# Optimization experiments

Measured on AMD Instinct MI355X. Metric: run time of the kernel, lower is better.

## Reference

```python
import jax, jax.numpy as jnp
import numpy as np

N, E, K = 10000, 160000, 5
K3 = K ** 3  # 125 spline kernel entries (kernel_size=5, dim=3)
NUM_CLASSES = 6890
# 8 corner combinations of the degree-1 open B-spline in 3 dims
_COMBOS = jnp.asarray(np.array([[i, j, k] for i in (0, 1) for j in (0, 1) for k in (0, 1)], dtype=np.int32))


def spline_basis(pseudo):
    # pseudo: [E,3] in [0,1]; degree-1 open B-spline, kernel_size K per dim
    p = pseudo * (K - 1)
    lo_f = jnp.floor(p)
    frac = p - lo_f                                   # [E,3]
    lo = jnp.clip(lo_f.astype(jnp.int32), 0, K - 1)    # [E,3]
    hi = jnp.minimum(lo + 1, K - 1)
    w = jnp.stack([1.0 - frac, frac], axis=-1)         # [E,3,2]
    idx = jnp.stack([lo, hi], axis=-1)                 # [E,3,2]
    c = _COMBOS                                        # [8,3]
    b = w[:, 0, c[:, 0]] * w[:, 1, c[:, 1]] * w[:, 2, c[:, 2]]          # [E,8]
    flat = idx[:, 0, c[:, 0]] + K * idx[:, 1, c[:, 1]] + K * K * idx[:, 2, c[:, 2]]  # [E,8]
    return b, flat


def spline_conv(x, src, dst, b, flat, W, root, bias):
    # x: [N,in], W: [K3,in,out], root: [in,out], bias: [out]
    xW = jnp.einsum('ni,kio->nko', x, W)               # [N,K3,out]
    gathered = xW[src[:, None], flat]                  # [E,8,out]
    msg = jnp.einsum('es,eso->eo', b, gathered)        # [E,out]
    agg = jax.ops.segment_sum(msg, dst, num_segments=N)
    deg = jax.ops.segment_sum(jnp.ones((msg.shape[0],), msg.dtype), dst, num_segments=N)
    agg = agg / jnp.maximum(deg, 1.0)[:, None]         # mean aggregation
    return agg + x @ root + bias


def setup_inputs() -> dict:
    key = jax.random.key(0)
    ks = jax.random.split(key, 24)
    s = 0.1
    x = jax.random.normal(ks[0], (N, 1), jnp.float32)
    edge_index = jax.random.randint(ks[1], (2, E), 0, N)
    pseudo = jax.random.uniform(ks[2], (E, 3), dtype=jnp.float32)
    W1 = jax.random.normal(ks[3], (K3, 1, 32), jnp.float32) * s
    root1 = jax.random.normal(ks[4], (1, 32), jnp.float32) * s
    b1 = jnp.zeros((32,), jnp.float32)
    W2 = jax.random.normal(ks[5], (K3, 32, 64), jnp.float32) * s
    root2 = jax.random.normal(ks[6], (32, 64), jnp.float32) * s
    b2 = jnp.zeros((64,), jnp.float32)
    Ws = jax.random.normal(ks[7], (4, K3, 64, 64), jnp.float32) * s  # convs 3-6
    roots = jax.random.normal(ks[8], (4, 64, 64), jnp.float32) * s
    bs = jnp.zeros((4, 64), jnp.float32)
    lin1_w = jax.random.normal(ks[9], (64, 256), jnp.float32) * s
    lin1_b = jnp.zeros((256,), jnp.float32)
    lin2_w = jax.random.normal(ks[10], (256, NUM_CLASSES), jnp.float32) * s
    lin2_b = jnp.zeros((NUM_CLASSES,), jnp.float32)
    return {'x': x, 'edge_index': edge_index, 'pseudo': pseudo,
            'W1': W1, 'root1': root1, 'b1': b1,
            'W2': W2, 'root2': root2, 'b2': b2,
            'Ws': Ws, 'roots': roots, 'bs': bs,
            'lin1_w': lin1_w, 'lin1_b': lin1_b, 'lin2_w': lin2_w, 'lin2_b': lin2_b}


def reference(x, edge_index, pseudo, W1, root1, b1, W2, root2, b2, Ws, roots, bs,
              lin1_w, lin1_b, lin2_w, lin2_b):
    src, dst = edge_index[0], edge_index[1]
    b, flat = spline_basis(pseudo)
    h = jax.nn.elu(spline_conv(x, src, dst, b, flat, W1, root1, b1))
    h = jax.nn.elu(spline_conv(h, src, dst, b, flat, W2, root2, b2))
    for l in range(4):  # convs 3-6, fixed layer loop
        h = jax.nn.elu(spline_conv(h, src, dst, b, flat, Ws[l], roots[l], bs[l]))
    h = jax.nn.elu(h @ lin1_w + lin1_b)
    # dropout is identity in eval mode
    logits = h @ lin2_w + lin2_b
    return jax.nn.log_softmax(logits, axis=-1)
```

## Files before the change

### kernel.cpp

```cpp
#include <hip/hip_runtime.h>
#include <hip/hip_bf16.h>
#include <math.h>

#define Nn 10000
#define Ee 160000
#define NPB 40
#define NBLK 250
#define NKER 125
#define NBUCK (NBLK * NKER)
#define KCHUNK 32

#define MPAD 10048
#define NPAD 6912
#define NCLS 6890

typedef short bf16x8 __attribute__((ext_vector_type(8)));
typedef float f32x4  __attribute__((ext_vector_type(4)));

__global__ __launch_bounds__(256) void basis_kernel(const float* __restrict__ pseudo,
                                                    float* __restrict__ bw,
                                                    int* __restrict__ fl)
{
    int e = blockIdx.x * 256 + threadIdx.x;
    if (e >= Ee) return;
    float p0 = pseudo[e * 3 + 0] * 4.f;
    float p1 = pseudo[e * 3 + 1] * 4.f;
    float p2 = pseudo[e * 3 + 2] * 4.f;
    float f0 = floorf(p0), f1 = floorf(p1), f2 = floorf(p2);
    float fr0 = p0 - f0, fr1 = p1 - f1, fr2 = p2 - f2;
    int lo0 = (int)f0; lo0 = lo0 < 0 ? 0 : (lo0 > 4 ? 4 : lo0);
    int lo1 = (int)f1; lo1 = lo1 < 0 ? 0 : (lo1 > 4 ? 4 : lo1);
    int lo2 = (int)f2; lo2 = lo2 < 0 ? 0 : (lo2 > 4 ? 4 : lo2);
    int hi0 = lo0 + 1 > 4 ? 4 : lo0 + 1;
    int hi1 = lo1 + 1 > 4 ? 4 : lo1 + 1;
    int hi2 = lo2 + 1 > 4 ? 4 : lo2 + 1;
#pragma unroll
    for (int s = 0; s < 8; ++s) {
        int c0 = (s >> 2) & 1, c1 = (s >> 1) & 1, c2 = s & 1;
        float b = (c0 ? fr0 : 1.f - fr0) * (c1 ? fr1 : 1.f - fr1) * (c2 ? fr2 : 1.f - fr2);
        int f = (c0 ? hi0 : lo0) + 5 * (c1 ? hi1 : lo1) + 25 * (c2 ? hi2 : lo2);
        bw[e * 8 + s] = b;
        fl[e * 8 + s] = f;
    }
}

__global__ __launch_bounds__(256) void deg_kernel(const int* __restrict__ dst, int* __restrict__ degi)
{
    int e = blockIdx.x * 256 + threadIdx.x;
    if (e >= Ee) return;
    atomicAdd(&degi[dst[e]], 1);
}

__global__ __launch_bounds__(256) void invdeg_kernel(const int* __restrict__ degi, float* __restrict__ invdeg)
{
    int n = blockIdx.x * 256 + threadIdx.x;
    if (n >= Nn) return;
    int d = degi[n];
    invdeg[n] = 1.f / (float)(d > 0 ? d : 1);
}

__global__ __launch_bounds__(256) void hist_kernel(const int* __restrict__ dst, const int* __restrict__ fl,
                                                   int* __restrict__ hist)
{
    int t = blockIdx.x * 256 + threadIdx.x;
    if (t >= Ee * 8) return;
    int e = t >> 3;
    int key = (dst[e] / NPB) * NKER + fl[t];
    atomicAdd(&hist[key], 1);
}

__global__ __launch_bounds__(1024) void scan_kernel(const int* __restrict__ hist, int* __restrict__ boff)
{
    const int T = 1024;
    const int per = (NBUCK + T - 1) / T;
    int t = threadIdx.x;
    int beg = t * per;
    int end = beg + per; if (end > NBUCK) end = NBUCK;
    int s = 0;
    for (int i = beg; i < end && i < NBUCK; ++i) s += hist[i];
    __shared__ int tmp[1024];
    tmp[t] = s;
    __syncthreads();
    for (int o2 = 1; o2 < 1024; o2 <<= 1) {
        int v = (t >= o2) ? tmp[t - o2] : 0;
        __syncthreads();
        tmp[t] += v;
        __syncthreads();
    }
    int run = tmp[t] - s;
    for (int i = beg; i < end && i < NBUCK; ++i) { boff[i] = run; run += hist[i]; }
    if (t == T - 1) boff[NBUCK] = run;
}

__global__ __launch_bounds__(256) void fill_kernel(const int* __restrict__ srcA, const int* __restrict__ dstA,
                                                   const float* __restrict__ bw, const int* __restrict__ fl,
                                                   int* __restrict__ cursor, uint2* __restrict__ recs)
{
    int t = blockIdx.x * 256 + threadIdx.x;
    if (t >= Ee * 8) return;
    int e = t >> 3;
    int d = dstA[e];
    int key = (d / NPB) * NKER + fl[t];
    int pos = atomicAdd(&cursor[key], 1);
    unsigned meta = (unsigned)srcA[e] | ((unsigned)(d % NPB) << 16);
    recs[pos] = make_uint2(meta, __float_as_uint(bw[t]));
}

template <int CIN, int COUT>
__global__ __launch_bounds__(256) void conv_pairs_kernel(const uint2* __restrict__ recs,
                                                         const int* __restrict__ boff,
                                                         const float* __restrict__ xin,
                                                         const float* __restrict__ W,
                                                         float* __restrict__ agg)
{
    __shared__ float aggl[NPB * COUT];
    const int blk = blockIdx.x;
    for (int idx = threadIdx.x; idx < NPB * COUT; idx += 256) aggl[idx] = 0.f;
    __syncthreads();

    const int lane = threadIdx.x & 63;
    const int wid  = threadIdx.x >> 6;
    const int o    = lane;

    int k0 = blockIdx.y * KCHUNK;
    int k1 = k0 + KCHUNK; if (k1 > NKER) k1 = NKER;

    for (int k = k0 + wid; k < k1; k += 4) {
        int bidx = blk * NKER + k;
        int pb = boff[bidx], pe = boff[bidx + 1];
        if (pb >= pe) continue;
        float wreg[CIN];
#pragma unroll
        for (int i = 0; i < CIN; ++i)
            wreg[i] = (o < COUT) ? W[(k * CIN + i) * COUT + o] : 0.f;

        for (int p = pb; p < pe; ++p) {
            uint2 r = recs[p];
            unsigned meta = (unsigned)__builtin_amdgcn_readfirstlane((int)r.x);
            float wt = __uint_as_float(r.y);
            int src = (int)(meta & 0xFFFFu);
            int dl  = (int)(meta >> 16);
            const float* xs = xin + src * CIN;
            float m0 = 0.f, m1 = 0.f, m2 = 0.f, m3 = 0.f;
            if (CIN >= 4) {
#pragma unroll
                for (int i = 0; i < CIN; i += 4) {
                    m0 += xs[i + 0] * wreg[i + 0];
                    m1 += xs[i + 1] * wreg[i + 1];
                    m2 += xs[i + 2] * wreg[i + 2];
                    m3 += xs[i + 3] * wreg[i + 3];
                }
            } else {
#pragma unroll
                for (int i = 0; i < CIN; ++i) m0 += xs[i] * wreg[i];
            }
            float m = (m0 + m1) + (m2 + m3);
            if (o < COUT) atomicAdd(&aggl[dl * COUT + o], wt * m);
        }
    }
    __syncthreads();
    for (int idx = threadIdx.x; idx < NPB * COUT; idx += 256) {
        int n = blk * NPB + idx / COUT;
        if (n < Nn) atomicAdd(&agg[n * COUT + (idx % COUT)], aggl[idx]);
    }
}

template <int CIN, int COUT>
__global__ __launch_bounds__(256) void epilogue_kernel(const float* __restrict__ agg,
                                                       const float* __restrict__ xin,
                                                       const float* __restrict__ root,
                                                       const float* __restrict__ bias,
                                                       const float* __restrict__ invdeg,
                                                       float* __restrict__ out)
{
    int idx = blockIdx.x * 256 + threadIdx.x;
    int n = idx / COUT, o = idx % COUT;
    if (n >= Nn) return;
    float r0 = 0.f, r1 = 0.f;
#pragma unroll
    for (int i = 0; i < CIN; i += 2) {
        r0 += xin[n * CIN + i] * root[i * COUT + o];
        if (CIN > 1) r1 += xin[n * CIN + i + 1] * root[(i + 1) * COUT + o];
    }
    float v = agg[n * COUT + o] * invdeg[n] + r0 + r1 + bias[o];
    out[n * COUT + o] = v > 0.f ? v : expm1f(v);
}

__global__ __launch_bounds__(256) void lin1_kernel(const float* __restrict__ h,
                                                   const float* __restrict__ w1,
                                                   const float* __restrict__ b1,
                                                   __hip_bfloat16* __restrict__ out)
{
    int n = blockIdx.x;
    __shared__ float hl[64];
    if (threadIdx.x < 64) hl[threadIdx.x] = h[n * 64 + threadIdx.x];
    __syncthreads();
    int j = threadIdx.x;
    float a0 = b1[j], a1 = 0.f, a2 = 0.f, a3 = 0.f;
#pragma unroll
    for (int i = 0; i < 64; i += 4) {
        a0 += hl[i + 0] * w1[(i + 0) * 256 + j];
        a1 += hl[i + 1] * w1[(i + 1) * 256 + j];
        a2 += hl[i + 2] * w1[(i + 2) * 256 + j];
        a3 += hl[i + 3] * w1[(i + 3) * 256 + j];
    }
    float acc = (a0 + a1) + (a2 + a3);
    float v = acc > 0.f ? acc : expm1f(acc);
    out[(size_t)n * 256 + j] = __float2bfloat16(v);
}

__global__ __launch_bounds__(256) void w2t_kernel(const float* __restrict__ w2,
                                                  __hip_bfloat16* __restrict__ w2t)
{
    __shared__ float t[32][33];
    int n0 = blockIdx.x * 32;
    int k0 = blockIdx.y * 32;
    int tx = threadIdx.x & 31, ty = threadIdx.x >> 5;
#pragma unroll
    for (int q = 0; q < 4; ++q) {
        int k = k0 + ty + 8 * q, n = n0 + tx;
        t[ty + 8 * q][tx] = (n < NCLS) ? w2[(size_t)k * NCLS + n] : 0.f;
    }
    __syncthreads();
#pragma unroll
    for (int q = 0; q < 4; ++q) {
        int n = n0 + ty + 8 * q;
        w2t[(size_t)n * 256 + k0 + tx] = __float2bfloat16(t[tx][ty + 8 * q]);
    }
}

__global__ __launch_bounds__(256) void lin2_mfma_kernel(const __hip_bfloat16* __restrict__ hbf,
                                                        const __hip_bfloat16* __restrict__ w2t,
                                                        const float* __restrict__ b2,
                                                        float* __restrict__ out)
{
    const int tid  = threadIdx.x;
    const int lane = tid & 63, wid = tid >> 6;
    const int wr = wid & 1, wc = wid >> 1;
    const int quad = lane >> 4, lq = lane & 15;

    const int mbase = blockIdx.x * 64 + wr * 32;
    const int nbase = blockIdx.y * 128 + wc * 64;

    f32x4 acc[2][4];
#pragma unroll
    for (int i = 0; i < 2; ++i)
#pragma unroll
        for (int j = 0; j < 4; ++j) acc[i][j] = (f32x4){0.f, 0.f, 0.f, 0.f};

    const unsigned short* A = (const unsigned short*)hbf;
    const unsigned short* B = (const unsigned short*)w2t;

    for (int kc = 0; kc < 256; kc += 32) {
        bf16x8 af[2], bfr[4];
#pragma unroll
        for (int mt = 0; mt < 2; ++mt)
            af[mt] = *(const bf16x8*)(A + (size_t)(mbase + mt * 16 + lq) * 256 + kc + quad * 8);
#pragma unroll
        for (int nt = 0; nt < 4; ++nt)
            bfr[nt] = *(const bf16x8*)(B + (size_t)(nbase + nt * 16 + lq) * 256 + kc + quad * 8);
#pragma unroll
        for (int mt = 0; mt < 2; ++mt)
#pragma unroll
            for (int nt = 0; nt < 4; ++nt)
                acc[mt][nt] = __builtin_amdgcn_mfma_f32_16x16x32_bf16(af[mt], bfr[nt], acc[mt][nt], 0, 0, 0);
    }

#pragma unroll
    for (int nt = 0; nt < 4; ++nt) {
        int col = nbase + nt * 16 + lq;
        if (col >= NCLS) continue;
        float bb = b2[col];
#pragma unroll
        for (int mt = 0; mt < 2; ++mt) {
#pragma unroll
            for (int r = 0; r < 4; ++r) {
                int row = mbase + mt * 16 + quad * 4 + r;
                if (row < Nn) out[(size_t)row * NCLS + col] = acc[mt][nt][r] + bb;
            }
        }
    }
}

__global__ __launch_bounds__(1024) void lsm_kernel(float* __restrict__ out)
{
    int row = blockIdx.x;
    float* p = out + (size_t)row * NCLS;
    __shared__ float red[16];
    int tid = threadIdx.x, lane = tid & 63, wid = tid >> 6;

    float m = -3.4e38f;
    for (int jj = tid; jj < NCLS; jj += 1024) m = fmaxf(m, p[jj]);
#pragma unroll
    for (int off = 32; off > 0; off >>= 1) m = fmaxf(m, __shfl_down(m, off));
    if (lane == 0) red[wid] = m;
    __syncthreads();
    if (tid == 0) {
        float mm = red[0];
        for (int w = 1; w < 16; ++w) mm = fmaxf(mm, red[w]);
        red[0] = mm;
    }
    __syncthreads();
    m = red[0];
    __syncthreads();

    float s = 0.f;
    for (int jj = tid; jj < NCLS; jj += 1024) s += expf(p[jj] - m);
#pragma unroll
    for (int off = 32; off > 0; off >>= 1) s += __shfl_down(s, off);
    if (lane == 0) red[wid] = s;
    __syncthreads();
    if (tid == 0) {
        float ss = 0.f;
        for (int w = 1; w < 16; ++w) ss += red[w];
        red[0] += ss;
    }
    __syncthreads();
    float lse = m + logf(red[0]);
    for (int jj = tid; jj < NCLS; jj += 1024) p[jj] -= lse;
}

extern "C" void kernel_launch(void* const* d_in, const int* in_sizes, int n_in,
                              void* d_out, int out_size, void* d_ws, size_t ws_size,
                              hipStream_t stream)
{
    const float* x      = (const float*)d_in[0];
    const int*   ei     = (const int*)d_in[1];
    const float* pseudo = (const float*)d_in[2];
    const float* W1     = (const float*)d_in[3];
    const float* root1  = (const float*)d_in[4];
    const float* b1     = (const float*)d_in[5];
    const float* W2     = (const float*)d_in[6];
    const float* root2  = (const float*)d_in[7];
    const float* b2     = (const float*)d_in[8];
    const float* Ws     = (const float*)d_in[9];
    const float* roots  = (const float*)d_in[10];
    const float* bs     = (const float*)d_in[11];
    const float* l1w    = (const float*)d_in[12];
    const float* l1b    = (const float*)d_in[13];
    const float* l2w    = (const float*)d_in[14];
    const float* l2b    = (const float*)d_in[15];
    float* out = (float*)d_out;

    const int* srcA = ei;
    const int* dstA = ei + Ee;

    char* base = (char*)d_ws;
    size_t off = 0;
    auto carve = [&](size_t bytes) -> void* {
        void* p = base + off;
        off += (bytes + 255) & ~(size_t)255;
        return p;
    };
    float* bw     = (float*)carve((size_t)Ee * 8 * 4);
    int*   fl     = (int*)carve((size_t)Ee * 8 * 4);
    int*   hist   = (int*)carve((size_t)NBUCK * 4);
    int*   boff   = (int*)carve((size_t)(NBUCK + 1) * 4);
    int*   cursor = (int*)carve((size_t)NBUCK * 4);
    uint2* recs   = (uint2*)carve((size_t)Ee * 8 * 8);
    int*   degi   = (int*)carve((size_t)Nn * 4);
    float* invdeg = (float*)carve((size_t)Nn * 4);
    float* agg    = (float*)carve((size_t)Nn * 64 * 4);
    float* hA     = (float*)carve((size_t)Nn * 64 * 4);
    float* hB     = (float*)carve((size_t)Nn * 64 * 4);
    __hip_bfloat16* hbf = (__hip_bfloat16*)carve((size_t)MPAD * 256 * 2);
    __hip_bfloat16* w2t = (__hip_bfloat16*)carve((size_t)NPAD * 256 * 2);
    (void)ws_size; (void)n_in; (void)in_sizes; (void)out_size;

    hipMemsetAsync(hist, 0, (size_t)NBUCK * 4, stream);
    hipMemsetAsync(degi, 0, (size_t)Nn * 4, stream);
    hipMemsetAsync(hbf, 0, (size_t)MPAD * 256 * 2, stream);

    basis_kernel<<<(Ee + 255) / 256, 256, 0, stream>>>(pseudo, bw, fl);
    deg_kernel<<<(Ee + 255) / 256, 256, 0, stream>>>(dstA, degi);
    invdeg_kernel<<<(Nn + 255) / 256, 256, 0, stream>>>(degi, invdeg);
    hist_kernel<<<(Ee * 8 + 255) / 256, 256, 0, stream>>>(dstA, fl, hist);
    scan_kernel<<<1, 1024, 0, stream>>>(hist, boff);
    hipMemcpyAsync(cursor, boff, (size_t)NBUCK * 4, hipMemcpyDeviceToDevice, stream);
    fill_kernel<<<(Ee * 8 + 255) / 256, 256, 0, stream>>>(srcA, dstA, bw, fl, cursor, recs);
    w2t_kernel<<<dim3((NPAD + 31) / 32, 8), 256, 0, stream>>>(l2w, w2t);

    const dim3 cgrid(NBLK, (NKER + KCHUNK - 1) / KCHUNK);

    hipMemsetAsync(agg, 0, (size_t)Nn * 64 * 4, stream);
    conv_pairs_kernel<1, 32><<<cgrid, 256, 0, stream>>>(recs, boff, x, W1, agg);
    epilogue_kernel<1, 32><<<(Nn * 32 + 255) / 256, 256, 0, stream>>>(agg, x, root1, b1, invdeg, hA);

    hipMemsetAsync(agg, 0, (size_t)Nn * 64 * 4, stream);
    conv_pairs_kernel<32, 64><<<cgrid, 256, 0, stream>>>(recs, boff, hA, W2, agg);
    epilogue_kernel<32, 64><<<(Nn * 64 + 255) / 256, 256, 0, stream>>>(agg, hA, root2, b2, invdeg, hB);

    float* cin = hB;
    float* cot = hA;
    for (int l = 0; l < 4; ++l) {
        hipMemsetAsync(agg, 0, (size_t)Nn * 64 * 4, stream);
        conv_pairs_kernel<64, 64><<<cgrid, 256, 0, stream>>>(recs, boff, cin, Ws + (size_t)l * 125 * 64 * 64, agg);
        epilogue_kernel<64, 64><<<(Nn * 64 + 255) / 256, 256, 0, stream>>>(
            agg, cin, roots + (size_t)l * 64 * 64, bs + (size_t)l * 64, invdeg, cot);
        float* t = cin; cin = cot; cot = t;
    }

    lin1_kernel<<<Nn, 256, 0, stream>>>(cin, l1w, l1b, hbf);
    lin2_mfma_kernel<<<dim3(MPAD / 64, NPAD / 128), 256, 0, stream>>>(hbf, w2t, l2b, out);
    lsm_kernel<<<Nn, 1024, 0, stream>>>(out);
}
```

Baseline: 3.466 ms.

## Remap spline conv so each lane handles one edge record and all outputs

The conv kernel now gives each lane its own edge record and has it compute every output channel, reading weights as wave-uniform scalar loads. Before, each lane owned one output channel and the wave walked the records one at a time. Shared-memory rows are padded by one float to spread atomics across banks, and block and chunk sizes change (50 nodes per block, 16 kernels per chunk). Each lane now holds up to 64 accumulators in registers, which adds register pressure and possibly spills. Lanes of a wave can also collide in shared-memory atomics when they share a destination.

```diff
diff --git a/kernel.cpp b/kernel.cpp
--- a/kernel.cpp
+++ b/kernel.cpp
@@ -4,11 +4,12 @@
 
 #define Nn 10000
 #define Ee 160000
-#define NPB 40
-#define NBLK 250
+#define NPB 50
+#define NBLK 200
 #define NKER 125
 #define NBUCK (NBLK * NKER)
-#define KCHUNK 32
+#define KCHUNK 16
+#define KS ((NKER + KCHUNK - 1) / KCHUNK)
 
 #define MPAD 10048
 #define NPAD 6912
@@ -107,61 +108,95 @@
 }
 
 template <int CIN, int COUT>
-__global__ __launch_bounds__(256) void conv_pairs_kernel(const uint2* __restrict__ recs,
-                                                         const int* __restrict__ boff,
-                                                         const float* __restrict__ xin,
-                                                         const float* __restrict__ W,
-                                                         float* __restrict__ agg)
-{
-    __shared__ float aggl[NPB * COUT];
+__global__ __launch_bounds__(256, 4) void conv_pairs_kernel(const uint2* __restrict__ recs,
+                                                            const int* __restrict__ boff,
+                                                            const float* __restrict__ xin,
+                                                            const float* __restrict__ W,
+                                                            float* __restrict__ agg)
+{
+    constexpr int STR = COUT + 1;
+    __shared__ float aggl[NPB * STR];
     const int blk = blockIdx.x;
-    for (int idx = threadIdx.x; idx < NPB * COUT; idx += 256) aggl[idx] = 0.f;
+    for (int idx = threadIdx.x; idx < NPB * STR; idx += 256) aggl[idx] = 0.f;
     __syncthreads();
 
     const int lane = threadIdx.x & 63;
     const int wid  = threadIdx.x >> 6;
-    const int o    = lane;
 
     int k0 = blockIdx.y * KCHUNK;
     int k1 = k0 + KCHUNK; if (k1 > NKER) k1 = NKER;
 
     for (int k = k0 + wid; k < k1; k += 4) {
-        int bidx = blk * NKER + k;
-        int pb = boff[bidx], pe = boff[bidx + 1];
+        const int kk = __builtin_amdgcn_readfirstlane(k);
+        const int bidx = blk * NKER + kk;
+        const int pb = boff[bidx], pe = boff[bidx + 1];
         if (pb >= pe) continue;
-        float wreg[CIN];
-#pragma unroll
-        for (int i = 0; i < CIN; ++i)
-            wreg[i] = (o < COUT) ? W[(k * CIN + i) * COUT + o] : 0.f;
-
-        for (int p = pb; p < pe; ++p) {
-            uint2 r = recs[p];
-            unsigned meta = (unsigned)__builtin_amdgcn_readfirstlane((int)r.x);
-            float wt = __uint_as_float(r.y);
-            int src = (int)(meta & 0xFFFFu);
-            int dl  = (int)(meta >> 16);
-            const float* xs = xin + src * CIN;
-            float m0 = 0.f, m1 = 0.f, m2 = 0.f, m3 = 0.f;
-            if (CIN >= 4) {
-#pragma unroll
+        const float* __restrict__ Wk = W + (size_t)kk * CIN * COUT;
+
+        for (int p = pb; p < pe; p += 64) {
+            const int j = p + lane;
+            const bool valid = j < pe;
+            uint2 r = recs[valid ? j : (pe - 1)];
+            const float wt = valid ? __uint_as_float(r.y) : 0.f;
+            const int src = (int)(r.x & 0xFFFFu);
+            const int dl  = (int)(r.x >> 16);
+            const float* __restrict__ xs = xin + (size_t)src * CIN;
+
+            float m[COUT];
+#pragma unroll
+            for (int o = 0; o < COUT; ++o) m[o] = 0.f;
+
+            if constexpr (CIN >= 4) {
+                f32x4 xc;
+                {
+                    f32x4 t0 = *(const f32x4*)(xs);
+                    xc[0] = t0[0] * wt; xc[1] = t0[1] * wt; xc[2] = t0[2] * wt; xc[3] = t0[3] * wt;
+                }
+#pragma unroll 1
                 for (int i = 0; i < CIN; i += 4) {
-                    m0 += xs[i + 0] * wreg[i + 0];
-                    m1 += xs[i + 1] * wreg[i + 1];
-                    m2 += xs[i + 2] * wreg[i + 2];
-                    m3 += xs[i + 3] * wreg[i + 3];
+                    f32x4 xn = {0.f, 0.f, 0.f, 0.f};
+                    if (i + 4 < CIN) {
+                        f32x4 t0 = *(const f32x4*)(xs + i + 4);
+                        xn[0] = t0[0] * wt; xn[1] = t0[1] * wt; xn[2] = t0[2] * wt; xn[3] = t0[3] * wt;
+                    }
+#pragma unroll
+                    for (int rr = 0; rr < 4; ++rr) {
+                        const float* __restrict__ wrow = Wk + (size_t)(i + rr) * COUT;
+#pragma unroll
+                        for (int ob = 0; ob < COUT; ob += 32) {
+                            float wr[32];
+#pragma unroll
+                            for (int t = 0; t < 32; ++t) wr[t] = wrow[ob + t];
+#pragma unroll
+                            for (int t = 0; t < 32; ++t) m[ob + t] += wr[t] * xc[rr];
+                        }
+                    }
+                    xc = xn;
                 }
             } else {
-#pragma unroll
-                for (int i = 0; i < CIN; ++i) m0 += xs[i] * wreg[i];
+                const float x0 = xs[0] * wt;
+#pragma unroll
+                for (int ob = 0; ob < COUT; ob += 32) {
+                    float wr[32];
+#pragma unroll
+                    for (int t = 0; t < 32; ++t) wr[t] = Wk[ob + t];
+#pragma unroll
+                    for (int t = 0; t < 32; ++t) m[ob + t] = wr[t] * x0;
+                }
             }
-            float m = (m0 + m1) + (m2 + m3);
-            if (o < COUT) atomicAdd(&aggl[dl * COUT + o], wt * m);
+
+            if (valid) {
+#pragma unroll
+                for (int o = 0; o < COUT; ++o)
+                    atomicAdd(&aggl[dl * STR + o], m[o]);
+            }
         }
     }
     __syncthreads();
     for (int idx = threadIdx.x; idx < NPB * COUT; idx += 256) {
-        int n = blk * NPB + idx / COUT;
-        if (n < Nn) atomicAdd(&agg[n * COUT + (idx % COUT)], aggl[idx]);
+        int dl = idx / COUT, o = idx % COUT;
+        int n = blk * NPB + dl;
+        atomicAdd(&agg[n * COUT + o], aggl[dl * STR + o]);
     }
 }
 
@@ -380,7 +415,7 @@
     fill_kernel<<<(Ee * 8 + 255) / 256, 256, 0, stream>>>(srcA, dstA, bw, fl, cursor, recs);
     w2t_kernel<<<dim3((NPAD + 31) / 32, 8), 256, 0, stream>>>(l2w, w2t);
 
-    const dim3 cgrid(NBLK, (NKER + KCHUNK - 1) / KCHUNK);
+    const dim3 cgrid(NBLK, KS);
 
     hipMemsetAsync(agg, 0, (size_t)Nn * 64 * 4, stream);
     conv_pairs_kernel<1, 32><<<cgrid, 256, 0, stream>>>(recs, boff, x, W1, agg);
```

Result: slower. 3.819 ms (+10.2%).

## Stage gathered edge features through LDS in batches with prefetch in spline conv

Applied to the files above, without the earlier changes.

The conv kernel now gathers a batch of B edge records cooperatively across the wavefront. Each record's source features are loaded with vector loads, pre-scaled by the basis weight and written to per-wave shared memory, and the next batch is prefetched while the current one is consumed. This replaces the old loop, where every lane issued scalar global loads for one edge at a time. Node blocks grow to 64 (shift/mask indexing), the kernel chunk shrinks to 16 and an occupancy hint is added, at the cost of more LDS use and extra register pressure.

```diff
diff --git a/kernel.cpp b/kernel.cpp
--- a/kernel.cpp
+++ b/kernel.cpp
@@ -4,11 +4,12 @@
 
 #define Nn 10000
 #define Ee 160000
-#define NPB 40
-#define NBLK 250
+#define NPB 64
+#define NBLK 157
 #define NKER 125
 #define NBUCK (NBLK * NKER)
-#define KCHUNK 32
+#define KCHUNK 16
+#define KS ((NKER + KCHUNK - 1) / KCHUNK)
 
 #define MPAD 10048
 #define NPAD 6912
@@ -65,7 +66,7 @@
     int t = blockIdx.x * 256 + threadIdx.x;
     if (t >= Ee * 8) return;
     int e = t >> 3;
-    int key = (dst[e] / NPB) * NKER + fl[t];
+    int key = (dst[e] >> 6) * NKER + fl[t];
     atomicAdd(&hist[key], 1);
 }
 
@@ -100,20 +101,27 @@
     if (t >= Ee * 8) return;
     int e = t >> 3;
     int d = dstA[e];
-    int key = (d / NPB) * NKER + fl[t];
+    int key = (d >> 6) * NKER + fl[t];
     int pos = atomicAdd(&cursor[key], 1);
-    unsigned meta = (unsigned)srcA[e] | ((unsigned)(d % NPB) << 16);
+    unsigned meta = (unsigned)srcA[e] | ((unsigned)(d & 63) << 16);
     recs[pos] = make_uint2(meta, __float_as_uint(bw[t]));
 }
 
-template <int CIN, int COUT>
-__global__ __launch_bounds__(256) void conv_pairs_kernel(const uint2* __restrict__ recs,
-                                                         const int* __restrict__ boff,
-                                                         const float* __restrict__ xin,
-                                                         const float* __restrict__ W,
-                                                         float* __restrict__ agg)
-{
+template <int CIN, int COUT, int B>
+__global__ __launch_bounds__(256, 3) void conv_pairs_kernel(const uint2* __restrict__ recs,
+                                                            const int* __restrict__ boff,
+                                                            const float* __restrict__ xin,
+                                                            const float* __restrict__ W,
+                                                            float* __restrict__ agg)
+{
+    constexpr int RSTR = (CIN >= 4) ? CIN + 4 : 2;
+    constexpr int LPR  = 64 / B;
+    constexpr int QC   = (CIN >= 4) ? (CIN / 4 / LPR) : 1;
+
     __shared__ float aggl[NPB * COUT];
+    __shared__ __align__(16) float xs_lds[4][B * RSTR];
+    __shared__ int dlb[4][(CIN >= 4) ? B : 1];
+
     const int blk = blockIdx.x;
     for (int idx = threadIdx.x; idx < NPB * COUT; idx += 256) aggl[idx] = 0.f;
     __syncthreads();
@@ -125,37 +133,91 @@
     int k0 = blockIdx.y * KCHUNK;
     int k1 = k0 + KCHUNK; if (k1 > NKER) k1 = NKER;
 
+    const int grow = lane & (B - 1);
+    const int gcb  = lane / B;
+
     for (int k = k0 + wid; k < k1; k += 4) {
-        int bidx = blk * NKER + k;
-        int pb = boff[bidx], pe = boff[bidx + 1];
+        const int kk = __builtin_amdgcn_readfirstlane(k);
+        const int bidx = blk * NKER + kk;
+        const int pb = boff[bidx], pe = boff[bidx + 1];
         if (pb >= pe) continue;
+
+        const float* __restrict__ Wk = W + (size_t)kk * CIN * COUT;
         float wreg[CIN];
 #pragma unroll
         for (int i = 0; i < CIN; ++i)
-            wreg[i] = (o < COUT) ? W[(k * CIN + i) * COUT + o] : 0.f;
-
-        for (int p = pb; p < pe; ++p) {
-            uint2 r = recs[p];
-            unsigned meta = (unsigned)__builtin_amdgcn_readfirstlane((int)r.x);
-            float wt = __uint_as_float(r.y);
-            int src = (int)(meta & 0xFFFFu);
-            int dl  = (int)(meta >> 16);
-            const float* xs = xin + src * CIN;
-            float m0 = 0.f, m1 = 0.f, m2 = 0.f, m3 = 0.f;
-            if (CIN >= 4) {
-#pragma unroll
-                for (int i = 0; i < CIN; i += 4) {
-                    m0 += xs[i + 0] * wreg[i + 0];
-                    m1 += xs[i + 1] * wreg[i + 1];
-                    m2 += xs[i + 2] * wreg[i + 2];
-                    m3 += xs[i + 3] * wreg[i + 3];
+            wreg[i] = (o < COUT) ? Wk[i * COUT + o] : 0.f;
+
+        const int cnt = pe - pb;
+        const int nb = (cnt + B - 1) / B;
+
+        f32x4 gx[QC];
+        float gx1 = 0.f;
+        float gwt = 0.f;
+        int   gdls = 0;
+
+        auto GATHER = [&](int b) {
+            int rid0 = pb + b * B + grow;
+            bool v = rid0 < pe;
+            uint2 rr = recs[v ? rid0 : (pe - 1)];
+            gwt = v ? __uint_as_float(rr.y) : 0.f;
+            int src = (int)(rr.x & 0xFFFFu);
+            gdls = (int)(rr.x >> 16) * COUT;
+            if constexpr (CIN >= 4) {
+                const f32x4* __restrict__ xr = (const f32x4*)(xin + (size_t)src * CIN);
+#pragma unroll
+                for (int q = 0; q < QC; ++q) gx[q] = xr[gcb * QC + q];
+            } else {
+                gx1 = xin[src];
+            }
+        };
+
+        auto STAGE = [&]() {
+            if constexpr (CIN >= 4) {
+                f32x4* __restrict__ xw = (f32x4*)&xs_lds[wid][grow * RSTR + gcb * QC * 4];
+#pragma unroll
+                for (int q = 0; q < QC; ++q) {
+                    f32x4 sv;
+                    sv[0] = gx[q][0] * gwt; sv[1] = gx[q][1] * gwt;
+                    sv[2] = gx[q][2] * gwt; sv[3] = gx[q][3] * gwt;
+                    xw[q] = sv;
+                }
+                if (gcb == 0) dlb[wid][grow] = gdls;
+            } else {
+                uint2* __restrict__ xw = (uint2*)&xs_lds[wid][0];
+                xw[grow] = make_uint2(__float_as_uint(gx1 * gwt), (unsigned)gdls);
+            }
+        };
+
+        GATHER(0);
+        for (int b = 0; b < nb; ++b) {
+            STAGE();
+            if (b + 1 < nb) GATHER(b + 1);
+            if constexpr (CIN >= 4) {
+#pragma unroll 2
+                for (int r = 0; r < B; ++r) {
+                    const f32x4* __restrict__ xv = (const f32x4*)&xs_lds[wid][r * RSTR];
+                    float m0 = 0.f, m1 = 0.f, m2 = 0.f, m3 = 0.f;
+#pragma unroll
+                    for (int c = 0; c < CIN / 4; ++c) {
+                        f32x4 x4 = xv[c];
+                        m0 = fmaf(x4[0], wreg[4 * c + 0], m0);
+                        m1 = fmaf(x4[1], wreg[4 * c + 1], m1);
+                        m2 = fmaf(x4[2], wreg[4 * c + 2], m2);
+                        m3 = fmaf(x4[3], wreg[4 * c + 3], m3);
+                    }
+                    float m = (m0 + m1) + (m2 + m3);
+                    int doff = dlb[wid][r];
+                    if (o < COUT) atomicAdd(&aggl[doff + o], m);
                 }
             } else {
-#pragma unroll
-                for (int i = 0; i < CIN; ++i) m0 += xs[i] * wreg[i];
+#pragma unroll 4
+                for (int r = 0; r < B; ++r) {
+                    uint2 q = ((const uint2*)&xs_lds[wid][0])[r];
+                    float m = __uint_as_float(q.x) * wreg[0];
+                    if (o < COUT) atomicAdd(&aggl[(int)q.y + o], m);
+                }
             }
-            float m = (m0 + m1) + (m2 + m3);
-            if (o < COUT) atomicAdd(&aggl[dl * COUT + o], wt * m);
         }
     }
     __syncthreads();
@@ -380,21 +442,21 @@
     fill_kernel<<<(Ee * 8 + 255) / 256, 256, 0, stream>>>(srcA, dstA, bw, fl, cursor, recs);
     w2t_kernel<<<dim3((NPAD + 31) / 32, 8), 256, 0, stream>>>(l2w, w2t);
 
-    const dim3 cgrid(NBLK, (NKER + KCHUNK - 1) / KCHUNK);
+    const dim3 cgrid(NBLK, KS);
 
     hipMemsetAsync(agg, 0, (size_t)Nn * 64 * 4, stream);
-    conv_pairs_kernel<1, 32><<<cgrid, 256, 0, stream>>>(recs, boff, x, W1, agg);
+    conv_pairs_kernel<1, 32, 64><<<cgrid, 256, 0, stream>>>(recs, boff, x, W1, agg);
     epilogue_kernel<1, 32><<<(Nn * 32 + 255) / 256, 256, 0, stream>>>(agg, x, root1, b1, invdeg, hA);
 
     hipMemsetAsync(agg, 0, (size_t)Nn * 64 * 4, stream);
-    conv_pairs_kernel<32, 64><<<cgrid, 256, 0, stream>>>(recs, boff, hA, W2, agg);
+    conv_pairs_kernel<32, 64, 32><<<cgrid, 256, 0, stream>>>(recs, boff, hA, W2, agg);
     epilogue_kernel<32, 64><<<(Nn * 64 + 255) / 256, 256, 0, stream>>>(agg, hA, root2, b2, invdeg, hB);
 
     float* cin = hB;
     float* cot = hA;
     for (int l = 0; l < 4; ++l) {
         hipMemsetAsync(agg, 0, (size_t)Nn * 64 * 4, stream);
-        conv_pairs_kernel<64, 64><<<cgrid, 256, 0, stream>>>(recs, boff, cin, Ws + (size_t)l * 125 * 64 * 64, agg);
+        conv_pairs_kernel<64, 64, 16><<<cgrid, 256, 0, stream>>>(recs, boff, cin, Ws + (size_t)l * 125 * 64 * 64, agg);
         epilogue_kernel<64, 64><<<(Nn * 64 + 255) / 256, 256, 0, stream>>>(
             agg, cin, roots + (size_t)l * 64 * 64, bs + (size_t)l * 64, invdeg, cot);
         float* t = cin; cin = cot; cot = t;
```

New measurement: 5.379 ms. 55.2% more time.
